# Optimization experiments

Hardware: AMD Instinct MI355X
Metric: run time of the kernel (lower is better)

## Reference

```python
import jax, jax.numpy as jnp
import numpy as np
from jax import lax

N, E, C, B, EF = 50000, 640000, 128, 64, 2
L = 32            # eval mode: 8 * num_virtual_tokens
D = 256           # mamba d_inner = expand * d_model
S = 128           # mamba d_state
R = 8             # dt_rank = ceil(C/16)
K = 4             # mamba d_conv


def _ln(x, g, b, eps=1e-5):
    m = x.mean(-1, keepdims=True)
    v = jnp.mean((x - m) ** 2, -1, keepdims=True)
    return (x - m) * lax.rsqrt(v + eps) * g + b


def setup_inputs() -> dict:
    key = jax.random.key(0)
    ks = iter(jax.random.split(key, 64))
    nrm = lambda sh, s=0.02: jax.random.normal(next(ks), sh, dtype=jnp.float32) * s
    inp = {}
    inp['x'] = jax.random.normal(next(ks), (N, C), dtype=jnp.float32)
    inp['edge_attr'] = jax.random.normal(next(ks), (E, EF), dtype=jnp.float32)
    inp['edge_index'] = jax.random.randint(next(ks), (2, E), 0, N, dtype=jnp.int32)
    inp['batch'] = jnp.sort(jax.random.randint(next(ks), (N,), 0, B, dtype=jnp.int32))
    # 8 spatial convs: edge-feature lift + node linear
    inp['We'] = nrm((8, EF, C), 0.1); inp['be'] = jnp.zeros((8, C))
    inp['Wc'] = nrm((8, C, C));       inp['bc'] = jnp.zeros((8, C))
    # GRUCell (torch gate order r,z,n)
    inp['Wih'] = nrm((C, 3 * C), 0.05); inp['Whh'] = nrm((C, 3 * C), 0.05)
    inp['bih'] = jnp.zeros((3 * C,));   inp['bhh'] = jnp.zeros((3 * C,))
    # Mamba
    inp['Win'] = nrm((C, 2 * D))
    inp['conv_w'] = nrm((D, K), 0.1); inp['conv_b'] = jnp.zeros((D,))
    inp['Wx'] = nrm((D, R + 2 * S))
    inp['Wdt'] = nrm((R, D), 0.1); inp['bdt'] = jnp.full((D,), -2.0)
    inp['A_log'] = jnp.log(jnp.tile(jnp.arange(1, S + 1, dtype=jnp.float32), (D, 1)))
    inp['Dp'] = jnp.ones((D,))
    inp['Wout'] = nrm((D, C))
    inp['g_m'] = jnp.ones((C,)); inp['b_m'] = jnp.zeros((C,))
    # merge MLP: Linear(9C->C) -> LN -> ReLU -> Linear(C->C)
    inp['Wm1'] = nrm((9 * C, C)); inp['bm1'] = jnp.zeros((C,))
    inp['g_h'] = jnp.ones((C,));  inp['b_h'] = jnp.zeros((C,))
    inp['Wm2'] = nrm((C, C));     inp['bm2'] = jnp.zeros((C,))
    inp['g_o'] = jnp.ones((C,));  inp['b_o'] = jnp.zeros((C,))
    return inp


def _forward(x, edge_attr, We, be, Wc, bc, Wih, Whh, bih, bhh, Win, conv_w, conv_b,
             Wx, Wdt, bdt, A_log, Dp, Wout, g_m, b_m, Wm1, bm1, g_h, b_h, Wm2, bm2,
             g_o, b_o, edge_index, batch):
    src, dst = edge_index[0], edge_index[1]
    # --- 8 graph convs (gather -> edge message -> scatter-add -> linear) ---
    xs = []
    x_src = x[src]                                        # [E,C]
    for i in range(8):
        msg = jax.nn.relu(x_src + edge_attr @ We[i] + be[i])
        agg = jax.ops.segment_sum(msg, dst, num_segments=N)
        xs.append(jax.nn.relu(agg @ Wc[i] + bc[i]))
    # --- to_dense_batch mean (zero-padded mean => segment_sum / maxN) ---
    counts = jax.ops.segment_sum(jnp.ones((N,), x.dtype), batch, num_segments=B)
    maxN = counts.max()
    x_mean = jax.ops.segment_sum(x, batch, num_segments=B) / maxN   # [B,C]
    # --- GRU virtual-token loop (input constant across steps) ---
    gi = x_mean @ Wih + bih
    ir, iz, inn = jnp.split(gi, 3, axis=-1)
    def gru_step(h, _):
        gh = h @ Whh + bhh
        hr, hz, hn = jnp.split(gh, 3, axis=-1)
        r = jax.nn.sigmoid(ir + hr)
        z = jax.nn.sigmoid(iz + hz)
        n = jnp.tanh(inn + r * hn)
        h = (1.0 - z) * n + z * h
        return h, h
    _, toks = lax.scan(gru_step, jnp.zeros((B, C), x.dtype), None, length=L)
    tokens = jnp.moveaxis(toks, 0, 1)                     # [B,L,C]
    # --- Mamba selective scan ---
    xz = tokens @ Win                                     # [B,L,2D]
    x_in, z_g = jnp.split(xz, 2, axis=-1)
    xp = jnp.pad(x_in, ((0, 0), (K - 1, 0), (0, 0)))      # causal depthwise conv
    x_c = sum(conv_w[:, k] * xp[:, k:k + L, :] for k in range(K)) + conv_b
    x_c = jax.nn.silu(x_c)                                # [B,L,D]
    dbl = x_c @ Wx
    dt_r, Bp, Cp = dbl[..., :R], dbl[..., R:R + S], dbl[..., R + S:]
    dt = jax.nn.softplus(dt_r @ Wdt + bdt)                # [B,L,D]
    A = -jnp.exp(A_log)                                   # [D,S]
    def ssm_step(h, inp):
        dt_t, B_t, C_t, x_t = inp                         # [B,D],[B,S],[B,S],[B,D]
        dA = jnp.exp(dt_t[..., None] * A)                 # [B,D,S]
        h = dA * h + (dt_t * x_t)[..., None] * B_t[:, None, :]
        y = jnp.einsum('bds,bs->bd', h, C_t)
        return h, y
    tm = lambda a: jnp.moveaxis(a, 1, 0)
    _, ys = lax.scan(ssm_step, jnp.zeros((B, D, S), x.dtype),
                     (tm(dt), tm(Bp), tm(Cp), tm(x_c)))
    y = jnp.moveaxis(ys, 0, 1) + Dp * x_c
    y = y * jax.nn.silu(z_g)
    mo = _ln(y @ Wout, g_m, b_m)                          # [B,L,C]
    x_m = mo[:, -1, :]
    x_m_node = x_m[batch]                                 # [N,C] gather
    # --- merge + residual + LN ---
    cat = jnp.concatenate(xs + [x_m_node], axis=-1)       # [N,9C]
    h1 = jax.nn.relu(_ln(cat @ Wm1 + bm1, g_h, b_h))
    x_new = h1 @ Wm2 + bm2
    return _ln(x + x_new, g_o, b_o)


def reference(x, edge_index, edge_attr, batch, We, be, Wc, bc, Wih, Whh, bih, bhh,
              Win, conv_w, conv_b, Wx, Wdt, bdt, A_log, Dp, Wout, g_m, b_m,
              Wm1, bm1, g_h, b_h, Wm2, bm2, g_o, b_o):
    return _forward(x, edge_attr, We, be, Wc, bc, Wih, Whh, bih, bhh, Win, conv_w,
                    conv_b, Wx, Wdt, bdt, A_log, Dp, Wout, g_m, b_m, Wm1, bm1,
                    g_h, b_h, Wm2, bm2, g_o, b_o, edge_index, batch)
```

## Files before the change

### kernel.cpp

```cpp
#include <hip/hip_runtime.h>
#include <hip/hip_bf16.h>

#define N_NODES 50000
#define N_EDGES 640000
#define C_DIM 128
#define B_DIM 64
#define L_DIM 32
#define D_DIM 256
#define S_DIM 128
#define R_DIM 8
#define K_CONV 4
#define NPW 4
#define NB 64
#define CHUNK_N 16704
#define SCAN_BLK 49

typedef unsigned short u16;
typedef __attribute__((ext_vector_type(8))) short bf16x8;
typedef __attribute__((ext_vector_type(4))) float f32x4;

__device__ __forceinline__ float bu2f(u16 u){ return __uint_as_float(((unsigned)u) << 16); }
__device__ __forceinline__ u16 f2bu(float f){
  __hip_bfloat16 h = __float2bfloat16(f);
  return *reinterpret_cast<u16*>(&h);
}
__device__ __forceinline__ float sigmoidf_(float x){ return 1.f/(1.f + expf(-x)); }
__device__ __forceinline__ int clampi(int v, int lo, int hi){ return max(lo, min(v, hi)); }
__device__ __forceinline__ float ldf(const void* p, size_t i, int f){
  return f ? bu2f(((const u16*)p)[i]) : ((const float*)p)[i];
}
__device__ __forceinline__ void stf(void* p, size_t i, int f, float v){
  if (f) ((u16*)p)[i] = f2bu(v); else ((float*)p)[i] = v;
}
__device__ __forceinline__ f32x4 mfma16(bf16x8 a, bf16x8 b, f32x4 c){
  return __builtin_amdgcn_mfma_f32_16x16x32_bf16(a, b, c, 0, 0, 0);
}
__device__ __forceinline__ float wave_sum64(float v){
  #pragma unroll
  for (int off = 32; off; off >>= 1) v += __shfl_xor(v, off);
  return v;
}

constexpr int K_SEG = 27;
constexpr int kCum[K_SEG+1] = {
  0, 2048, 3072, 134144, 135168, 184320, 233472, 233856, 234240, 299776,
  300800, 301056, 368640, 370688, 370944, 403712, 403968, 436736, 436864,
  436992, 584448, 584576, 584704, 584832, 601216, 601344, 601472, 601600 };
#define ARENA_TOTAL 601600

struct Ptrs { const void* p[K_SEG]; };


__global__ void detect_kernel(const unsigned* dp_bits, const unsigned* cand1,
                              const unsigned* cand2, int* flags){
  int lane = threadIdx.x & 63;
  unsigned idx = (unsigned)((lane * 9973u) % (unsigned)N_EDGES);
  int v1 = (cand1[idx] < (unsigned)N_NODES) ? 1 : 0;
  int v2 = (cand2[idx] < (unsigned)N_NODES) ? 1 : 0;
  unsigned long long m1 = __ballot(v1);
  unsigned long long m2 = __ballot(v2);
  if (lane == 0){
    flags[0] = (dp_bits[0] == 0x3F803F80u) ? 1 : 0;
    flags[1] = (__popcll(m1) > __popcll(m2)) ? 1 : 0;
  }
}


__global__ __launch_bounds__(256) void cvt_all_kernel(Ptrs ptrs, float* arena,
                                                      const int* flags){
  int i = blockIdx.x*256 + threadIdx.x;
  if (i >= ARENA_TOTAL) return;
  int lo = 0, hi = K_SEG;
  #pragma unroll
  for (int it = 0; it < 5; it++){
    int mid = (lo + hi) >> 1;
    if (i >= kCum[mid]) lo = mid; else hi = mid;
  }
  int elem = i - kCum[lo];
  const void* sp = ptrs.p[lo];
  arena[i] = flags[0] ? bu2f(((const u16*)sp)[elem]) : ((const float*)sp)[elem];
}


__global__ __launch_bounds__(256) void wtrans_kernel(
    const float* __restrict__ WcF, const float* __restrict__ Wm1F,
    const float* __restrict__ Wm2F,
    u16* __restrict__ WcT_hi, u16* __restrict__ WcT_lo,
    u16* __restrict__ Wm1T_hi, u16* __restrict__ Wm1T_lo,
    u16* __restrict__ Wm2T_hi, u16* __restrict__ Wm2T_lo)
{
  int i = blockIdx.x*256 + threadIdx.x;
  if (i >= 8*C_DIM*C_DIM) return;
  int h = i >> 14, j = (i >> 7) & 127, k = i & 127;
  {
    float w = WcF[(h<<14) + (k<<7) + j];
    u16 hi = f2bu(w); u16 lo = f2bu(w - bu2f(hi));
    WcT_hi[i] = hi; WcT_lo[i] = lo;
  }
  {
    float w = Wm1F[((size_t)((h<<7) + k) << 7) + j];
    u16 hi = f2bu(w); u16 lo = f2bu(w - bu2f(hi));
    Wm1T_hi[i] = hi; Wm1T_lo[i] = lo;
  }
  if (i < C_DIM*C_DIM){
    int j2 = i >> 7, k2 = i & 127;
    float w = Wm2F[(k2<<7) + j2];
    u16 hi = f2bu(w); u16 lo = f2bu(w - bu2f(hi));
    Wm2T_hi[i] = hi; Wm2T_lo[i] = lo;
  }
}


__global__ void hist_kernel(const int* __restrict__ eiA, const int* __restrict__ eiB,
                            const int* __restrict__ flags, int* __restrict__ hist){
  const int* dst = (flags[1] ? eiA : eiB) + N_EDGES;
  int e = blockIdx.x*256 + threadIdx.x;
  if (e >= N_EDGES) return;
  int d = clampi(dst[e], 0, N_NODES-1);
  atomicAdd(&hist[d], 1);
}

__global__ __launch_bounds__(1024) void scan1_kernel(const int* __restrict__ hist,
                                                     int* __restrict__ tmp,
                                                     int* __restrict__ bsums){
  __shared__ int buf[1024];
  int b = blockIdx.x, tid = threadIdx.x;
  int i = b*1024 + tid;
  int v = (i < N_NODES) ? hist[i] : 0;
  buf[tid] = v;
  __syncthreads();
  for (int off = 1; off < 1024; off <<= 1){
    int t = (tid >= off) ? buf[tid-off] : 0;
    __syncthreads();
    buf[tid] += t;
    __syncthreads();
  }
  if (i < N_NODES) tmp[i] = buf[tid];
  if (tid == 1023) bsums[b] = buf[1023];
}

__global__ void scan2_kernel(int* __restrict__ bsums, int* __restrict__ offsets){
  if (threadIdx.x == 0){
    int run = 0;
    for (int b = 0; b < SCAN_BLK; b++){ int v = bsums[b]; bsums[b] = run; run += v; }
    offsets[N_NODES] = run;
  }
}

__global__ __launch_bounds__(1024) void scan3_kernel(int* __restrict__ offsets,
                                                     int* __restrict__ hist,
                                                     const int* __restrict__ bsums){
  int b = blockIdx.x, tid = threadIdx.x;
  int i = b*1024 + tid;
  if (i >= N_NODES) return;
  int incl = offsets[i];
  int h = hist[i];
  int excl = incl - h + bsums[b];
  offsets[i] = excl;
  hist[i] = excl;
}

__global__ void perm_kernel(const void* __restrict__ in1, const void* __restrict__ in2,
                            const int* __restrict__ flags, int* __restrict__ cursor,
                            int* __restrict__ sortedSrc, float2* __restrict__ sortedEA){
  int e = blockIdx.x*256 + threadIdx.x;
  if (e >= N_EDGES) return;
  const int f1 = flags[1], f = flags[0];
  const int* ei  = (const int*)(f1 ? in1 : in2);
  const void* eav = f1 ? in2 : in1;
  int d = clampi(ei[N_EDGES + e], 0, N_NODES-1);
  int s = clampi(ei[e], 0, N_NODES-1);
  float a0, a1;
  if (f){ const u16* e16 = (const u16*)eav; a0 = bu2f(e16[2*e]); a1 = bu2f(e16[2*e+1]); }
  else  { const float* e32 = (const float*)eav; a0 = e32[2*e]; a1 = e32[2*e+1]; }
  int pos = atomicAdd(&cursor[d], 1);
  pos = clampi(pos, 0, N_EDGES-1);
  sortedSrc[pos] = s;
  sortedEA[pos] = make_float2(a0, a1);
}


__global__ __launch_bounds__(256, 8) void gather_kernel(
    const void* __restrict__ xv, const int* __restrict__ sortedSrc,
    const float2* __restrict__ sortedEA, const int* __restrict__ offsets,
    const float* __restrict__ WeF, const float* __restrict__ beF,
    const int* __restrict__ flags, u16* __restrict__ aggBuf,
    int n0, int ncnt)
{
  int w = blockIdx.x*4 + (threadIdx.x >> 6);
  int nsets = (ncnt + NPW - 1) / NPW;
  if (w >= 2*nsets) return;
  int chalf = w & 1;
  int nset = w >> 1;
  int lane = threadIdx.x & 63;
  int c = lane + chalf*64;
  const int f = flags[0];
  const u16* x16 = (const u16*)xv; const float* x32 = (const float*)xv;

  float we0[8], we1[8], beh[8];
  #pragma unroll
  for (int h = 0; h < 8; h++){
    we0[h] = WeF[h*2*C_DIM + c];
    we1[h] = WeF[h*2*C_DIM + C_DIM + c];
    beh[h] = beF[h*C_DIM + c];
  }

  auto LD = [&](int q, float& xr, float2& er){
    int s = sortedSrc[q];
    er = sortedEA[q];
    int idx = s*C_DIM + c;
    xr = f ? bu2f(x16[idx]) : x32[idx];
  };

  int nl_end = min(nset*NPW + NPW, ncnt);
  for (int nl = nset*NPW; nl < nl_end; nl++){
    int n = n0 + nl;
    int q0 = offsets[n];
    int cnt = offsets[n+1] - q0;

    float acc[8] = {0,0,0,0,0,0,0,0};
    float xA=0.f, xB=0.f, xC=0.f, xD=0.f;
    float2 eA=make_float2(0,0), eB=make_float2(0,0), eC=make_float2(0,0), eD=make_float2(0,0);
    if (cnt > 0) LD(q0+0, xA, eA);
    if (cnt > 1) LD(q0+1, xB, eB);
    if (cnt > 2) LD(q0+2, xC, eC);
    if (cnt > 3) LD(q0+3, xD, eD);

    for (int j = 0; j < cnt; j += 4){
      float ux0=xA, ux1=xB, ux2=xC, ux3=xD;
      float2 ue0=eA, ue1=eB, ue2=eC, ue3=eD;
      if (j+4 < cnt) LD(q0+j+4, xA, eA);
      if (j+5 < cnt) LD(q0+j+5, xB, eB);
      if (j+6 < cnt) LD(q0+j+6, xC, eC);
      if (j+7 < cnt) LD(q0+j+7, xD, eD);
      #pragma unroll
      for (int h = 0; h < 8; h++)
        acc[h] += fmaxf(fmaf(ue0.x, we0[h], fmaf(ue0.y, we1[h], ux0 + beh[h])), 0.f);
      if (j+1 < cnt){
        #pragma unroll
        for (int h = 0; h < 8; h++)
          acc[h] += fmaxf(fmaf(ue1.x, we0[h], fmaf(ue1.y, we1[h], ux1 + beh[h])), 0.f);
      }
      if (j+2 < cnt){
        #pragma unroll
        for (int h = 0; h < 8; h++)
          acc[h] += fmaxf(fmaf(ue2.x, we0[h], fmaf(ue2.y, we1[h], ux2 + beh[h])), 0.f);
      }
      if (j+3 < cnt){
        #pragma unroll
        for (int h = 0; h < 8; h++)
          acc[h] += fmaxf(fmaf(ue3.x, we0[h], fmaf(ue3.y, we1[h], ux3 + beh[h])), 0.f);
      }
    }

    int base = nl*2048 + c;
    #pragma unroll
    for (int h = 0; h < 8; h++){
      u16 hv = f2bu(acc[h]);
      u16 lv = f2bu(acc[h] - bu2f(hv));
      aggBuf[base + h*256]       = hv;
      aggBuf[base + h*256 + 128] = lv;
    }
  }
}


__global__ __launch_bounds__(128) void pool_kernel(
    const void* __restrict__ xv, const int* __restrict__ batch,
    float* __restrict__ xsum, int* __restrict__ counts, const int* __restrict__ flags)
{
  int c = threadIdx.x;
  int f = flags[0];
  int n0 = blockIdx.x * 32;
  int nend = min(n0 + 32, N_NODES);
  float acc = 0.f; int cnt = 0;
  int curb = clampi(batch[n0], 0, B_DIM-1);
  for (int n = n0; n < nend; n++){
    int b = clampi(batch[n], 0, B_DIM-1);
    if (b != curb){
      atomicAdd(&xsum[curb*C_DIM + c], acc);
      if (c == 0) atomicAdd(&counts[curb], cnt);
      acc = 0.f; cnt = 0; curb = b;
    }
    acc += ldf(xv, (size_t)n*C_DIM + c, f);
    cnt++;
  }
  atomicAdd(&xsum[curb*C_DIM + c], acc);
  if (c == 0) atomicAdd(&counts[curb], cnt);
}


__global__ __launch_bounds__(384, 1) void gru_kernel(
    const float* __restrict__ xsum, const int* __restrict__ counts,
    const float* __restrict__ Wih, const float* __restrict__ bih,
    const float* __restrict__ Whh, const float* __restrict__ bhh,
    float* __restrict__ tokens)
{
  int b = blockIdx.x, j = threadIdx.x;
  __shared__ float xm[C_DIM], h[C_DIM], gh[3*C_DIM], sgi[3*C_DIM];
  __shared__ float mxS;
  if (j == 0){
    int m = 1;
    for (int bb = 0; bb < B_DIM; bb++) m = max(m, counts[bb]);
    mxS = (float)m;
  }
  __syncthreads();
  if (j < C_DIM){ xm[j] = xsum[b*C_DIM + j] / mxS; h[j] = 0.f; }
  __syncthreads();

  {
    float a0=0.f, a1=0.f, a2=0.f, a3=0.f;
    for (int k = 0; k < C_DIM; k += 4){
      a0 = fmaf(xm[k],   Wih[(k  )*384 + j], a0);
      a1 = fmaf(xm[k+1], Wih[(k+1)*384 + j], a1);
      a2 = fmaf(xm[k+2], Wih[(k+2)*384 + j], a2);
      a3 = fmaf(xm[k+3], Wih[(k+3)*384 + j], a3);
    }
    sgi[j] = bih[j] + ((a0 + a1) + (a2 + a3));
  }

  float w[C_DIM];
  #pragma unroll
  for (int k = 0; k < C_DIM; k++) w[k] = Whh[k*384 + j];
  float bh = bhh[j];
  __syncthreads();

  float g_ir = 0.f, g_iz = 0.f, g_in = 0.f;
  if (j < C_DIM){ g_ir = sgi[j]; g_iz = sgi[C_DIM + j]; g_in = sgi[2*C_DIM + j]; }

  for (int t = 0; t < L_DIM; t++){
    float a0=0.f, a1=0.f, a2=0.f, a3=0.f;
    #pragma unroll
    for (int k = 0; k < C_DIM; k += 4){
      a0 = fmaf(h[k],   w[k],   a0);
      a1 = fmaf(h[k+1], w[k+1], a1);
      a2 = fmaf(h[k+2], w[k+2], a2);
      a3 = fmaf(h[k+3], w[k+3], a3);
    }
    gh[j] = bh + ((a0 + a1) + (a2 + a3));
    __syncthreads();
    if (j < C_DIM){
      float r  = sigmoidf_(g_ir + gh[j]);
      float z  = sigmoidf_(g_iz + gh[C_DIM + j]);
      float nn = tanhf(g_in + r*gh[2*C_DIM + j]);
      float hn = (1.f - z)*nn + z*h[j];
      h[j] = hn;
      tokens[((size_t)b*L_DIM + t)*C_DIM + j] = hn;
    }
    __syncthreads();
  }
}


__global__ __launch_bounds__(256) void token_proj_kernel(
    const float* __restrict__ tokens, const float* __restrict__ Win,
    float* __restrict__ x_in, float* __restrict__ z_last)
{
  int row = blockIdx.x;
  int d = threadIdx.x;
  __shared__ float tok[C_DIM];
  if (d < C_DIM) tok[d] = tokens[(size_t)row*C_DIM + d];
  __syncthreads();
  float acc = 0.f;
  for (int k = 0; k < C_DIM; k++) acc = fmaf(tok[k], Win[k*512 + d], acc);
  x_in[(size_t)row*D_DIM + d] = acc;
  if ((row & (L_DIM-1)) == L_DIM-1){
    float acc2 = 0.f;
    for (int k = 0; k < C_DIM; k++) acc2 = fmaf(tok[k], Win[k*512 + D_DIM + d], acc2);
    z_last[(row >> 5)*D_DIM + d] = acc2;
  }
}


__global__ __launch_bounds__(256) void xproj_kernel(
    const float* __restrict__ x_in, const float* __restrict__ cw,
    const float* __restrict__ cb, const float* __restrict__ Wx,
    const float* __restrict__ Wdt, const float* __restrict__ bdt,
    float* __restrict__ dt, float* __restrict__ Bp, float* __restrict__ Cp,
    float* __restrict__ x_c)
{
  int row = blockIdx.x; int tid = threadIdx.x;
  int t = row & (L_DIM-1);
  __shared__ float xr[D_DIM];
  __shared__ float dtr[R_DIM];
  float acc0 = cb[tid];
  #pragma unroll
  for (int k = 0; k < K_CONV; k++){
    int tt = t + k - (K_CONV-1);
    if (tt >= 0) acc0 = fmaf(cw[tid*K_CONV + k], x_in[(size_t)(row + tt - t)*D_DIM + tid], acc0);
  }
  float xcv = acc0 * sigmoidf_(acc0);
  x_c[(size_t)row*D_DIM + tid] = xcv;
  xr[tid] = xcv;
  __syncthreads();
  float acc = 0.f;
  #pragma unroll 4
  for (int k = 0; k < D_DIM; k++) acc = fmaf(xr[k], Wx[k*264 + tid], acc);
  if (tid < R_DIM)              dtr[tid] = acc;
  else if (tid < R_DIM+S_DIM)   Bp[(size_t)row*S_DIM + tid - R_DIM] = acc;
  else                          Cp[(size_t)row*S_DIM + tid - (R_DIM+S_DIM)] = acc;
  if (tid < 264 - D_DIM){
    float acc2 = 0.f;
    #pragma unroll 4
    for (int k = 0; k < D_DIM; k++) acc2 = fmaf(xr[k], Wx[k*264 + D_DIM + tid], acc2);
    Cp[(size_t)row*S_DIM + (D_DIM - (R_DIM+S_DIM)) + tid] = acc2;
  }
  __syncthreads();
  float a = bdt[tid];
  #pragma unroll
  for (int r = 0; r < R_DIM; r++) a = fmaf(dtr[r], Wdt[r*D_DIM + tid], a);
  dt[(size_t)row*D_DIM + tid] = (a > 20.f) ? a : log1pf(expf(a));
}


__global__ __launch_bounds__(256) void ssm_kernel(
    const float* __restrict__ dt, const float* __restrict__ Bp,
    const float* __restrict__ Cp, const float* __restrict__ x_c,
    const float* __restrict__ A_log, const float* __restrict__ Dp_,
    const float* __restrict__ z_last, float* __restrict__ y_last)
{
  int wid = (blockIdx.x*256 + threadIdx.x) >> 6;
  int lane = threadIdx.x & 63;
  int b = wid >> 8, d = wid & (D_DIM-1);
  int s0 = lane*2;
  float A0 = -expf(A_log[d*S_DIM + s0]);
  float A1 = -expf(A_log[d*S_DIM + s0 + 1]);
  float h0 = 0.f, h1 = 0.f;
  for (int t = 0; t < L_DIM; t++){
    int row = b*L_DIM + t;
    float dtv = dt[(size_t)row*D_DIM + d];
    float xv  = x_c[(size_t)row*D_DIM + d];
    float bx = dtv * xv;
    float2 Bv = ((const float2*)(Bp + (size_t)row*S_DIM))[lane];
    h0 = fmaf(expf(dtv*A0), h0, bx*Bv.x);
    h1 = fmaf(expf(dtv*A1), h1, bx*Bv.y);
  }
  int row = b*L_DIM + (L_DIM-1);
  float2 Cv = ((const float2*)(Cp + (size_t)row*S_DIM))[lane];
  float y = h0*Cv.x + h1*Cv.y;
  #pragma unroll
  for (int off = 32; off; off >>= 1) y += __shfl_down(y, off);
  if (lane == 0){
    float xc = x_c[(size_t)row*D_DIM + d];
    float yv = y + Dp_[d]*xc;
    float z  = z_last[b*D_DIM + d];
    yv *= z * sigmoidf_(z);
    y_last[b*D_DIM + d] = yv;
  }
}


__device__ __forceinline__ float block_sum_128(float v, float* red){
  int c = threadIdx.x;
  red[c] = v; __syncthreads();
  if (c < 64) red[c] += red[c+64];
  __syncthreads();
  if (c < 64){
    float r = red[c];
    #pragma unroll
    for (int off = 32; off; off >>= 1) r += __shfl_down(r, off);
    if (c == 0) red[0] = r;
  }
  __syncthreads();
  float out = red[0];
  __syncthreads();
  return out;
}

__global__ __launch_bounds__(128) void xm_kernel(
    const float* __restrict__ y_last, const float* __restrict__ Wout,
    const float* __restrict__ g_m, const float* __restrict__ b_m,
    const float* __restrict__ Wm1x, float* __restrict__ proj)
{
  int b = blockIdx.x, c = threadIdx.x;
  __shared__ float yr[D_DIM];
  __shared__ float red[C_DIM];
  __shared__ float xmr[C_DIM];
  yr[c]        = y_last[b*D_DIM + c];
  yr[C_DIM+c]  = y_last[b*D_DIM + C_DIM + c];
  __syncthreads();
  float acc = 0.f;
  for (int k = 0; k < D_DIM; k++) acc = fmaf(yr[k], Wout[k*C_DIM + c], acc);
  float mean = block_sum_128(acc, red) * (1.f/C_DIM);
  float dv = acc - mean;
  float var = block_sum_128(dv*dv, red) * (1.f/C_DIM);
  float mo = dv*rsqrtf(var + 1e-5f)*g_m[c] + b_m[c];
  xmr[c] = mo;
  __syncthreads();
  float p = 0.f;
  for (int k = 0; k < C_DIM; k++) p = fmaf(xmr[k], Wm1x[k*C_DIM + c], p);
  proj[b*C_DIM + c] = p;
}


__global__ __launch_bounds__(256, 2) void fused_kernel(
    const void* __restrict__ xv, const u16* __restrict__ aggBuf, int n0, int ncnt,
    const u16* __restrict__ WcT_hi, const u16* __restrict__ WcT_lo,
    const float* __restrict__ bcF,
    const u16* __restrict__ Wm1T_hi, const u16* __restrict__ Wm1T_lo,
    const float* __restrict__ bm1F, const float* __restrict__ proj,
    const int* __restrict__ batch,
    const float* __restrict__ ghF, const float* __restrict__ bhF,
    const u16* __restrict__ Wm2T_hi, const u16* __restrict__ Wm2T_lo,
    const float* __restrict__ bm2F,
    const float* __restrict__ goF, const float* __restrict__ boF,
    const int* __restrict__ flags, void* __restrict__ out)
{
  __shared__ __align__(16) char smem[65536];
  float* pS = (float*)smem;

  const int tid = threadIdx.x;
  const int f = flags[0];
  const u16* x16 = (const u16*)xv; const float* x32 = (const float*)xv;
  const int lbase = blockIdx.x * NB;
  const int nbase = n0 + lbase;

  const int lane = tid & 63;
  const int wv = tid >> 6;
  const int m16 = lane & 15;
  const int lg = lane >> 4;
  const int colbase = wv * 32;
  const int jA = colbase + m16;

  int ahoff[4], aoff[4];
  #pragma unroll
  for (int kk = 0; kk < 4; kk++){
    int sw = (m16 & 7) << 4;
    ahoff[kk] = m16*512 + ((kk*64 + lg*16) ^ sw);
    aoff[kk]  = m16*256 + ((kk*64 + lg*16) ^ sw);
  }

  int sg_node[8], sg_u[8], sg_dst[8];
  #pragma unroll
  for (int j = 0; j < 8; j++){
    int i = tid + j*256;
    int t = i >> 9, g = (i >> 5) & 15, u = i & 31;
    sg_node[j] = lbase + t*16 + g;
    sg_u[j] = u << 4;
    sg_dst[j] = t*8192 + (((i & 511) << 4) ^ ((g & 7) << 4));
  }

  bf16x8 sreg[8];
  auto stage_load = [&](int h){
    #pragma unroll
    for (int j = 0; j < 8; j++)
      sreg[j] = *(const bf16x8*)((const char*)aggBuf +
                 (((size_t)sg_node[j]*8 + h) << 9) + sg_u[j]);
  };
  auto stage_commit = [&](){
    #pragma unroll
    for (int j = 0; j < 8; j++) *(bf16x8*)(smem + sg_dst[j]) = sreg[j];
  };
  auto LDW = [&](const u16* Whi, const u16* Wlo, int h, bf16x8 (*w)[4]){
    #pragma unroll
    for (int kk = 0; kk < 4; kk++){
      size_t bi0 = ((size_t)(h*C_DIM + jA) << 7) + kk*32 + lg*8;
      w[kk][0] = *(const bf16x8*)(Whi + bi0);
      w[kk][1] = *(const bf16x8*)(Wlo + bi0);
      w[kk][2] = *(const bf16x8*)(Whi + bi0 + 2048);
      w[kk][3] = *(const bf16x8*)(Wlo + bi0 + 2048);
    }
  };

  stage_load(0);
  stage_commit();
  __syncthreads();

  f32x4 P0[4], P1[4];
  #pragma unroll
  for (int t = 0; t < 4; t++){
    P0[t] = (f32x4){0,0,0,0};
    P1[t] = (f32x4){0,0,0,0};
  }

  bf16x8 w[4][4];
  for (int h = 0; h < 8; h++){
    const bool pf = (h+1 < 8);
    LDW(WcT_hi, WcT_lo, h, w);
    if (pf) stage_load(h+1);
    float bc0 = bcF[h*C_DIM + colbase + m16];
    float bc1 = bcF[h*C_DIM + colbase + 16 + m16];

    #pragma unroll
    for (int t = 0; t < 4; t++){
      f32x4 a0 = {0,0,0,0}, a1 = {0,0,0,0};
      #pragma unroll
      for (int kk = 0; kk < 4; kk++){
        bf16x8 ah = *(const bf16x8*)(smem + t*8192 + ahoff[kk]);
        bf16x8 al = *(const bf16x8*)(smem + t*8192 + ahoff[kk] + 256);
        a0 = mfma16(ah, w[kk][0], a0);
        a0 = mfma16(ah, w[kk][1], a0);
        a0 = mfma16(al, w[kk][0], a0);
        a1 = mfma16(ah, w[kk][2], a1);
        a1 = mfma16(ah, w[kk][3], a1);
        a1 = mfma16(al, w[kk][2], a1);
      }
      #pragma unroll
      for (int r = 0; r < 4; r++){
        int row = lg*4 + r;
        int rs = row*256;
        int sw2 = (row & 7) << 4;
        {
          float v = fmaxf(a0[r] + bc0, 0.f);
          u16 hi = f2bu(v); u16 lo = f2bu(v - bu2f(hi));
          int bo = rs + (((colbase + m16)*2) ^ sw2);
          *(u16*)(smem + 32768 + t*8192 + bo) = hi;
          *(u16*)(smem + 32768 + t*8192 + 4096 + bo) = lo;
        }
        {
          float v = fmaxf(a1[r] + bc1, 0.f);
          u16 hi = f2bu(v); u16 lo = f2bu(v - bu2f(hi));
          int bo = rs + (((colbase + 16 + m16)*2) ^ sw2);
          *(u16*)(smem + 32768 + t*8192 + bo) = hi;
          *(u16*)(smem + 32768 + t*8192 + 4096 + bo) = lo;
        }
      }
    }
    if (pf) stage_commit();
    LDW(Wm1T_hi, Wm1T_lo, h, w);
    __syncthreads();

    #pragma unroll
    for (int t = 0; t < 4; t++){
      #pragma unroll
      for (int kk = 0; kk < 4; kk++){
        bf16x8 yh = *(const bf16x8*)(smem + 32768 + t*8192 + aoff[kk]);
        bf16x8 yl = *(const bf16x8*)(smem + 32768 + t*8192 + 4096 + aoff[kk]);
        P0[t] = mfma16(yh, w[kk][0], P0[t]);
        P0[t] = mfma16(yh, w[kk][1], P0[t]);
        P0[t] = mfma16(yl, w[kk][0], P0[t]);
        P1[t] = mfma16(yh, w[kk][2], P1[t]);
        P1[t] = mfma16(yh, w[kk][3], P1[t]);
        P1[t] = mfma16(yl, w[kk][2], P1[t]);
      }
    }
    __syncthreads();
  }

  #pragma unroll
  for (int t = 0; t < 4; t++){
    #pragma unroll
    for (int r = 0; r < 4; r++){
      int row = t*16 + lg*4 + r;
      pS[row*C_DIM + colbase + m16]      = P0[t][r];
      pS[row*C_DIM + colbase + 16 + m16] = P1[t][r];
    }
  }
  __syncthreads();

  for (int g = 0; g < 16; g++){
    int n_l = wv*16 + g;
    int nc = min(nbase + n_l, N_NODES-1);
    int bi = clampi(batch[nc], 0, B_DIM-1);
    float v0 = pS[n_l*C_DIM + lane]      + bm1F[lane]      + proj[bi*C_DIM + lane];
    float v1 = pS[n_l*C_DIM + 64 + lane] + bm1F[64 + lane] + proj[bi*C_DIM + 64 + lane];
    float mean = wave_sum64(v0 + v1) * (1.f/C_DIM);
    float d0 = v0 - mean, d1 = v1 - mean;
    float var = wave_sum64(d0*d0 + d1*d1) * (1.f/C_DIM);
    float rinv = rsqrtf(var + 1e-5f);
    float h0 = fmaxf(d0*rinv*ghF[lane]      + bhF[lane], 0.f);
    float h1v = fmaxf(d1*rinv*ghF[64+lane]  + bhF[64+lane], 0.f);
    int sw3 = (n_l & 7) << 4;
    {
      u16 hi = f2bu(h0); u16 lo = f2bu(h0 - bu2f(hi));
      int bo = n_l*256 + ((lane*2) ^ sw3);
      *(u16*)(smem + 32768 + bo) = hi;
      *(u16*)(smem + 49152 + bo) = lo;
    }
    {
      u16 hi = f2bu(h1v); u16 lo = f2bu(h1v - bu2f(hi));
      int bo = n_l*256 + (((64+lane)*2) ^ sw3);
      *(u16*)(smem + 32768 + bo) = hi;
      *(u16*)(smem + 49152 + bo) = lo;
    }
  }
  LDW(Wm2T_hi, Wm2T_lo, 0, w);
  __syncthreads();

  {
    f32x4 A0[4], A1[4];
    #pragma unroll
    for (int t = 0; t < 4; t++){
      A0[t] = (f32x4){0,0,0,0};
      A1[t] = (f32x4){0,0,0,0};
      #pragma unroll
      for (int kk = 0; kk < 4; kk++){
        bf16x8 yh = *(const bf16x8*)(smem + 32768 + t*4096 + aoff[kk]);
        bf16x8 yl = *(const bf16x8*)(smem + 49152 + t*4096 + aoff[kk]);
        A0[t] = mfma16(yh, w[kk][0], A0[t]);
        A0[t] = mfma16(yh, w[kk][1], A0[t]);
        A0[t] = mfma16(yl, w[kk][0], A0[t]);
        A1[t] = mfma16(yh, w[kk][2], A1[t]);
        A1[t] = mfma16(yh, w[kk][3], A1[t]);
        A1[t] = mfma16(yl, w[kk][2], A1[t]);
      }
    }
    __syncthreads();
    #pragma unroll
    for (int t = 0; t < 4; t++){
      #pragma unroll
      for (int r = 0; r < 4; r++){
        int row = t*16 + lg*4 + r;
        pS[row*C_DIM + colbase + m16]      = A0[t][r];
        pS[row*C_DIM + colbase + 16 + m16] = A1[t][r];
      }
    }
  }
  __syncthreads();

  for (int g = 0; g < 16; g++){
    int n_l = wv*16 + g;
    int n = nbase + n_l;
    int nc = min(n, N_NODES-1);
    float x0 = f ? bu2f(x16[(size_t)nc*C_DIM + lane])      : x32[(size_t)nc*C_DIM + lane];
    float x1 = f ? bu2f(x16[(size_t)nc*C_DIM + 64 + lane]) : x32[(size_t)nc*C_DIM + 64 + lane];
    float v0 = pS[n_l*C_DIM + lane]      + bm2F[lane]      + x0;
    float v1 = pS[n_l*C_DIM + 64 + lane] + bm2F[64 + lane] + x1;
    float mean = wave_sum64(v0 + v1) * (1.f/C_DIM);
    float d0 = v0 - mean, d1 = v1 - mean;
    float var = wave_sum64(d0*d0 + d1*d1) * (1.f/C_DIM);
    float rinv = rsqrtf(var + 1e-5f);
    if (n_l < ncnt){
      stf(out, (size_t)n*C_DIM + lane,      f, d0*rinv*goF[lane]      + boF[lane]);
      stf(out, (size_t)n*C_DIM + 64 + lane, f, d1*rinv*goF[64+lane]   + boF[64+lane]);
    }
  }
}


extern "C" void kernel_launch(void* const* d_in, const int* in_sizes, int n_in,
                              void* d_out, int out_size, void* d_ws, size_t ws_size,
                              hipStream_t stream)
{
  const void* x      = d_in[0];
  const void* in1    = d_in[1];
  const void* in2    = d_in[2];
  const int*  batch  = (const int*)d_in[3];
  (void)in_sizes; (void)n_in; (void)out_size; (void)ws_size;

  char* ws = (char*)d_ws;
  size_t off = 0;
  auto alloc = [&](size_t nbytes)->char*{
    char* p = ws + off;
    off += (nbytes + 255) & ~(size_t)255;
    return p;
  };
  int*   flags = (int*)alloc(8);
  float* arena = (float*)alloc((size_t)ARENA_TOTAL*4);
  int* hist    = (int*)alloc((size_t)N_NODES*4);
  int* offsets = (int*)alloc((size_t)(N_NODES+1)*4);
  int* bsums   = (int*)alloc((size_t)SCAN_BLK*4);
  int* sortedSrc = (int*)alloc((size_t)N_EDGES*4);
  float2* sortedEA = (float2*)alloc((size_t)N_EDGES*8);
  float* proj   = (float*)alloc((size_t)B_DIM*C_DIM*4);
  float* xsum   = (float*)alloc((size_t)B_DIM*C_DIM*4);
  int*   counts = (int*)alloc((size_t)B_DIM*4);
  float* tokens = (float*)alloc((size_t)B_DIM*L_DIM*C_DIM*4);
  float* x_in   = (float*)alloc((size_t)B_DIM*L_DIM*D_DIM*4);
  float* x_c    = (float*)alloc((size_t)B_DIM*L_DIM*D_DIM*4);
  float* Cp     = (float*)alloc((size_t)B_DIM*L_DIM*S_DIM*4);
  float* z_last = (float*)alloc((size_t)B_DIM*D_DIM*4);
  float* y_last = (float*)alloc((size_t)B_DIM*D_DIM*4);
  u16* WcT_hi  = (u16*)alloc((size_t)8*C_DIM*C_DIM*2);
  u16* WcT_lo  = (u16*)alloc((size_t)8*C_DIM*C_DIM*2);
  u16* Wm1T_hi = (u16*)alloc((size_t)8*C_DIM*C_DIM*2);
  u16* Wm1T_lo = (u16*)alloc((size_t)8*C_DIM*C_DIM*2);
  u16* Wm2T_hi = (u16*)alloc((size_t)C_DIM*C_DIM*2);
  u16* Wm2T_lo = (u16*)alloc((size_t)C_DIM*C_DIM*2);
  u16* aggBuf  = (u16*)alloc((size_t)CHUNK_N*8*256*2);
  float* Bp  = tokens;
  float* dtb = x_in;

  float* WeF   = arena + 0;      float* beF   = arena + 2048;
  float* WcF   = arena + 3072;   float* bcF   = arena + 134144;
  float* WihF  = arena + 135168; float* WhhF  = arena + 184320;
  float* bihF  = arena + 233472; float* bhhF  = arena + 233856;
  float* WinF  = arena + 234240; float* cwF   = arena + 299776;
  float* cbF   = arena + 300800; float* WxF   = arena + 301056;
  float* WdtF  = arena + 368640; float* bdtF  = arena + 370688;
  float* AlF   = arena + 370944; float* DpF   = arena + 403712;
  float* WoutF = arena + 403968; float* gmF   = arena + 436736;
  float* bmF   = arena + 436864; float* Wm1F  = arena + 436992;
  float* bm1F  = arena + 584448; float* ghF   = arena + 584576;
  float* bhF   = arena + 584704; float* Wm2F  = arena + 584832;
  float* bm2F  = arena + 601216; float* goF   = arena + 601344;
  float* boF   = arena + 601472;

  detect_kernel<<<1, 64, 0, stream>>>((const unsigned*)d_in[19],
                                      (const unsigned*)in1, (const unsigned*)in2, flags);

  Ptrs ptrs;
  for (int i = 0; i < K_SEG; i++) ptrs.p[i] = d_in[4 + i];
  cvt_all_kernel<<<(ARENA_TOTAL + 255)/256, 256, 0, stream>>>(ptrs, arena, flags);
  wtrans_kernel<<<(8*C_DIM*C_DIM + 255)/256, 256, 0, stream>>>(
      WcF, Wm1F, Wm2F, WcT_hi, WcT_lo, Wm1T_hi, Wm1T_lo, Wm2T_hi, Wm2T_lo);

  hipMemsetAsync(hist, 0, (size_t)N_NODES*4, stream);
  hist_kernel<<<(N_EDGES + 255)/256, 256, 0, stream>>>((const int*)in1, (const int*)in2, flags, hist);
  scan1_kernel<<<SCAN_BLK, 1024, 0, stream>>>(hist, offsets, bsums);
  scan2_kernel<<<1, 64, 0, stream>>>(bsums, offsets);
  scan3_kernel<<<SCAN_BLK, 1024, 0, stream>>>(offsets, hist, bsums);
  perm_kernel<<<(N_EDGES + 255)/256, 256, 0, stream>>>(in1, in2, flags, hist, sortedSrc, sortedEA);

  hipMemsetAsync(xsum, 0, (size_t)B_DIM*C_DIM*4 + 256, stream);
  pool_kernel<<<(N_NODES + 31)/32, 128, 0, stream>>>(x, batch, xsum, counts, flags);
  gru_kernel<<<B_DIM, 384, 0, stream>>>(xsum, counts, WihF, bihF, WhhF, bhhF, tokens);
  token_proj_kernel<<<B_DIM*L_DIM, 256, 0, stream>>>(tokens, WinF, x_in, z_last);
  xproj_kernel<<<B_DIM*L_DIM, 256, 0, stream>>>(x_in, cwF, cbF, WxF, WdtF, bdtF, dtb, Bp, Cp, x_c);
  ssm_kernel<<<(B_DIM*D_DIM)/4, 256, 0, stream>>>(dtb, Bp, Cp, x_c, AlF, DpF, z_last, y_last);
  xm_kernel<<<B_DIM, 128, 0, stream>>>(y_last, WoutF, gmF, bmF, Wm1F + 8*C_DIM*C_DIM, proj);

  for (int n0 = 0; n0 < N_NODES; n0 += CHUNK_N){
    int ncnt = min(CHUNK_N, N_NODES - n0);
    int nsets = (ncnt + NPW - 1) / NPW;
    int nwaves = 2 * nsets;
    gather_kernel<<<(nwaves + 3)/4, 256, 0, stream>>>(
        x, sortedSrc, sortedEA, offsets, WeF, beF, flags, aggBuf, n0, ncnt);
    fused_kernel<<<(ncnt + NB - 1)/NB, 256, 0, stream>>>(
        x, aggBuf, n0, ncnt, WcT_hi, WcT_lo, bcF, Wm1T_hi, Wm1T_lo, bm1F,
        proj, batch, ghF, bhF, Wm2T_hi, Wm2T_lo, bm2F, goF, boF, flags, d_out);
  }
}
```

Baseline: 942.3 us.

## Pack sorted edge records into 16-byte structs and size chunks from workspace

Merges the separate sorted source-index and edge-attribute arrays into one 16-byte aligned record, so each gathered edge needs a single vector load instead of two scattered loads. The aggregation buffer chunk size is now derived from the available workspace, up to the whole graph, which cuts the number of gather/fused launch pairs and the tail effects of chunking. It also changes a bounds check in the fused kernel to use lbase. The cost is a padding word per edge that raises edge-record traffic by a third, and a larger aggregation buffer.

```diff
diff --git a/kernel.cpp b/kernel.cpp
--- a/kernel.cpp
+++ b/kernel.cpp
@@ -12,12 +12,14 @@
 #define K_CONV 4
 #define NPW 4
 #define NB 64
-#define CHUNK_N 16704
+#define MAX_CHUNK 50048
 #define SCAN_BLK 49
 
 typedef unsigned short u16;
 typedef __attribute__((ext_vector_type(8))) short bf16x8;
 typedef __attribute__((ext_vector_type(4))) float f32x4;
+
+struct __align__(16) ERec { int s; float a0, a1; int pad; };
 
 __device__ __forceinline__ float bu2f(u16 u){ return __uint_as_float(((unsigned)u) << 16); }
 __device__ __forceinline__ u16 f2bu(float f){
@@ -162,7 +164,7 @@
 
 __global__ void perm_kernel(const void* __restrict__ in1, const void* __restrict__ in2,
                             const int* __restrict__ flags, int* __restrict__ cursor,
-                            int* __restrict__ sortedSrc, float2* __restrict__ sortedEA){
+                            ERec* __restrict__ sortedRec){
   int e = blockIdx.x*256 + threadIdx.x;
   if (e >= N_EDGES) return;
   const int f1 = flags[1], f = flags[0];
@@ -175,14 +177,14 @@
   else  { const float* e32 = (const float*)eav; a0 = e32[2*e]; a1 = e32[2*e+1]; }
   int pos = atomicAdd(&cursor[d], 1);
   pos = clampi(pos, 0, N_EDGES-1);
-  sortedSrc[pos] = s;
-  sortedEA[pos] = make_float2(a0, a1);
+  ERec r; r.s = s; r.a0 = a0; r.a1 = a1; r.pad = 0;
+  sortedRec[pos] = r;
 }
 
 
 __global__ __launch_bounds__(256, 8) void gather_kernel(
-    const void* __restrict__ xv, const int* __restrict__ sortedSrc,
-    const float2* __restrict__ sortedEA, const int* __restrict__ offsets,
+    const void* __restrict__ xv, const ERec* __restrict__ sortedRec,
+    const int* __restrict__ offsets,
     const float* __restrict__ WeF, const float* __restrict__ beF,
     const int* __restrict__ flags, u16* __restrict__ aggBuf,
     int n0, int ncnt)
@@ -206,9 +208,9 @@
   }
 
   auto LD = [&](int q, float& xr, float2& er){
-    int s = sortedSrc[q];
-    er = sortedEA[q];
-    int idx = s*C_DIM + c;
+    ERec r = sortedRec[q];
+    er = make_float2(r.a0, r.a1);
+    int idx = r.s*C_DIM + c;
     xr = f ? bu2f(x16[idx]) : x32[idx];
   };
 
@@ -720,7 +722,7 @@
     float d0 = v0 - mean, d1 = v1 - mean;
     float var = wave_sum64(d0*d0 + d1*d1) * (1.f/C_DIM);
     float rinv = rsqrtf(var + 1e-5f);
-    if (n_l < ncnt){
+    if (lbase + n_l < ncnt){
       stf(out, (size_t)n*C_DIM + lane,      f, d0*rinv*goF[lane]      + boF[lane]);
       stf(out, (size_t)n*C_DIM + 64 + lane, f, d1*rinv*goF[64+lane]   + boF[64+lane]);
     }
@@ -736,7 +738,7 @@
   const void* in1    = d_in[1];
   const void* in2    = d_in[2];
   const int*  batch  = (const int*)d_in[3];
-  (void)in_sizes; (void)n_in; (void)out_size; (void)ws_size;
+  (void)in_sizes; (void)n_in; (void)out_size;
 
   char* ws = (char*)d_ws;
   size_t off = 0;
@@ -750,8 +752,7 @@
   int* hist    = (int*)alloc((size_t)N_NODES*4);
   int* offsets = (int*)alloc((size_t)(N_NODES+1)*4);
   int* bsums   = (int*)alloc((size_t)SCAN_BLK*4);
-  int* sortedSrc = (int*)alloc((size_t)N_EDGES*4);
-  float2* sortedEA = (float2*)alloc((size_t)N_EDGES*8);
+  ERec* sortedRec = (ERec*)alloc((size_t)N_EDGES*16);
   float* proj   = (float*)alloc((size_t)B_DIM*C_DIM*4);
   float* xsum   = (float*)alloc((size_t)B_DIM*C_DIM*4);
   int*   counts = (int*)alloc((size_t)B_DIM*4);
@@ -767,7 +768,15 @@
   u16* Wm1T_lo = (u16*)alloc((size_t)8*C_DIM*C_DIM*2);
   u16* Wm2T_hi = (u16*)alloc((size_t)C_DIM*C_DIM*2);
   u16* Wm2T_lo = (u16*)alloc((size_t)C_DIM*C_DIM*2);
-  u16* aggBuf  = (u16*)alloc((size_t)CHUNK_N*8*256*2);
+
+  size_t avail = (ws_size > off + 4096) ? (ws_size - off - 4096) : 0;
+  long long cn = (long long)(avail / 4096);
+  cn &= ~63LL;
+  if (cn > MAX_CHUNK) cn = MAX_CHUNK;
+  if (cn < 64) cn = 16704;
+  const int chunkN = (int)cn;
+  u16* aggBuf = (u16*)alloc((size_t)chunkN * 4096);
+
   float* Bp  = tokens;
   float* dtb = x_in;
 
@@ -800,7 +809,7 @@
   scan1_kernel<<<SCAN_BLK, 1024, 0, stream>>>(hist, offsets, bsums);
   scan2_kernel<<<1, 64, 0, stream>>>(bsums, offsets);
   scan3_kernel<<<SCAN_BLK, 1024, 0, stream>>>(offsets, hist, bsums);
-  perm_kernel<<<(N_EDGES + 255)/256, 256, 0, stream>>>(in1, in2, flags, hist, sortedSrc, sortedEA);
+  perm_kernel<<<(N_EDGES + 255)/256, 256, 0, stream>>>(in1, in2, flags, hist, sortedRec);
 
   hipMemsetAsync(xsum, 0, (size_t)B_DIM*C_DIM*4 + 256, stream);
   pool_kernel<<<(N_NODES + 31)/32, 128, 0, stream>>>(x, batch, xsum, counts, flags);
@@ -810,12 +819,12 @@
   ssm_kernel<<<(B_DIM*D_DIM)/4, 256, 0, stream>>>(dtb, Bp, Cp, x_c, AlF, DpF, z_last, y_last);
   xm_kernel<<<B_DIM, 128, 0, stream>>>(y_last, WoutF, gmF, bmF, Wm1F + 8*C_DIM*C_DIM, proj);
 
-  for (int n0 = 0; n0 < N_NODES; n0 += CHUNK_N){
-    int ncnt = min(CHUNK_N, N_NODES - n0);
+  for (int n0 = 0; n0 < N_NODES; n0 += chunkN){
+    int ncnt = min(chunkN, N_NODES - n0);
     int nsets = (ncnt + NPW - 1) / NPW;
     int nwaves = 2 * nsets;
     gather_kernel<<<(nwaves + 3)/4, 256, 0, stream>>>(
-        x, sortedSrc, sortedEA, offsets, WeF, beF, flags, aggBuf, n0, ncnt);
+        x, sortedRec, offsets, WeF, beF, flags, aggBuf, n0, ncnt);
     fused_kernel<<<(ncnt + NB - 1)/NB, 256, 0, stream>>>(
         x, aggBuf, n0, ncnt, WcT_hi, WcT_lo, bcF, Wm1T_hi, Wm1T_lo, bm1F,
         proj, batch, ghF, bhF, Wm2T_hi, Wm2T_lo, bm2F, goF, boF, flags, d_out);
```

New measurement: 786.2 us. -16.6%, faster.
